# Performance work log

Measured on AMD Instinct MI355X. Metric: run time of the kernel, lower is better.

Reference implementation:

```python
import jax, jax.numpy as jnp
import numpy as np

H = 16   # n_heads == n_I
D = 64   # d_q = d_k = d_v = d_r
DX = H * D
B, S = 4, 2048

def setup_inputs() -> dict:
    key = jax.random.key(0)
    ks = jax.random.split(key, 9)
    sc = 0.02
    return {
        "value": jax.random.normal(ks[0], (B, S, DX), jnp.float32),
        "key":   jax.random.normal(ks[1], (B, S, DX), jnp.float32),
        "query": jax.random.normal(ks[2], (B, S, DX), jnp.float32),
        "Wq_w": jax.random.normal(ks[3], (DX, DX), jnp.float32) * sc,
        "Wq_b": jnp.zeros((DX,), jnp.float32),
        "Wk_w": jax.random.normal(ks[4], (DX, DX), jnp.float32) * sc,
        "Wk_b": jnp.zeros((DX,), jnp.float32),
        "Wv_w": jax.random.normal(ks[5], (DX, DX), jnp.float32) * sc,
        "Wv_b": jnp.zeros((DX,), jnp.float32),
        "Wr_w": jax.random.normal(ks[6], (DX, DX), jnp.float32) * sc,
        "Wr_b": jnp.zeros((DX,), jnp.float32),
        "Wout_w": jax.random.normal(ks[7], (DX, DX), jnp.float32) * sc,
        "Wout_b": jnp.zeros((DX,), jnp.float32),
    }

def _heads(x, b, s):
    # [b, s, H*D] -> [b, H, s, D]
    return x.reshape(b, s, H, D).transpose(0, 2, 1, 3)

def reference(value, key, query, Wq_w, Wq_b, Wk_w, Wk_b, Wv_w, Wv_b,
              Wr_w, Wr_b, Wout_w, Wout_b):
    b, s, _ = query.shape
    # torch nn.Linear: y = x @ W.T + b
    Q = _heads(query @ Wq_w.T + Wq_b, b, s)   # [b,H,s,D]
    K = _heads(key   @ Wk_w.T + Wk_b, b, s)
    V = _heads(value @ Wv_w.T + Wv_b, b, s)
    R = _heads(query @ Wr_w.T + Wr_b, b, s)
    dot_scale = jnp.sqrt(jnp.float32(D))
    scores = jnp.einsum("bhid,bhjd->bhij", Q, K) / dot_scale  # [b,H,s,s]
    attn = jax.nn.softmax(scores, axis=-1)                    # dropout p=0
    out = jnp.einsum("bhij,bhjd->bhid", attn, V)              # [b,H,s,D]
    out = out * R                                             # R-gating
    out = out.transpose(0, 2, 1, 3).reshape(b, s, H * D)
    return out @ Wout_w.T + Wout_b
```

## Files before the change

### kernel.cpp

```cpp
#include <hip/hip_runtime.h>
#include <hip/hip_bf16.h>

typedef __bf16 bf16;
typedef __bf16 bf16x4 __attribute__((ext_vector_type(4)));
typedef __bf16 bf16x8 __attribute__((ext_vector_type(8)));
typedef float  f32x4  __attribute__((ext_vector_type(4)));

#define MFMA_16x16x32(a, b, c) __builtin_amdgcn_mfma_f32_16x16x32_bf16((a), (b), (c), 0, 0, 0)

typedef const void __attribute__((address_space(1))) gvoid;
typedef void __attribute__((address_space(3))) svoid;

__device__ __forceinline__ void async_copy16(const void* gptr, void* ldsptr) {
    __builtin_amdgcn_global_load_lds((gvoid*)gptr, (svoid*)ldsptr, 16, 0, 0);
}

__device__ __forceinline__ int swz8(int row, int quad) {
    return (quad ^ ((row >> 1) & 3)) * 8;
}

__global__ void cvt3_acts(const float* __restrict__ s0, const float* __restrict__ s1,
                          const float* __restrict__ s2,
                          bf16* __restrict__ d0, bf16* __restrict__ d1, bf16* __restrict__ d2)
{
    constexpr int N4SEG = 8192 * 1024 / 4;
    int i = blockIdx.x * blockDim.x + threadIdx.x;
    const int stride = gridDim.x * blockDim.x;
    for (; i < 3 * N4SEG; i += stride) {
        const int seg = i / N4SEG;
        const int j = i - seg * N4SEG;
        const float* s = seg == 0 ? s0 : (seg == 1 ? s1 : s2);
        bf16* d = seg == 0 ? d0 : (seg == 1 ? d1 : d2);
        float4 v = ((const float4*)s)[j];
        bf16x4 o = { (bf16)v.x, (bf16)v.y, (bf16)v.z, (bf16)v.w };
        ((bf16x4*)d)[j] = o;
    }
}

__global__ void cvt5_wts(const float* __restrict__ s0, const float* __restrict__ s1,
                         const float* __restrict__ s2, const float* __restrict__ s3,
                         const float* __restrict__ s4,
                         bf16* __restrict__ d0, bf16* __restrict__ d1, bf16* __restrict__ d2,
                         bf16* __restrict__ d3, bf16* __restrict__ d4)
{
    constexpr int N4SEG = 1024 * 1024 / 4;
    int i = blockIdx.x * blockDim.x + threadIdx.x;
    const int stride = gridDim.x * blockDim.x;
    for (; i < 5 * N4SEG; i += stride) {
        const int seg = i / N4SEG;
        const int j = i - seg * N4SEG;
        const float* s = seg == 0 ? s0 : seg == 1 ? s1 : seg == 2 ? s2 : seg == 3 ? s3 : s4;
        bf16* d = seg == 0 ? d0 : seg == 1 ? d1 : seg == 2 ? d2 : seg == 3 ? d3 : d4;
        float4 v = ((const float4*)s)[j];
        bf16x4 o = { (bf16)v.x, (bf16)v.y, (bf16)v.z, (bf16)v.w };
        ((bf16x4*)d)[j] = o;
    }
}

__global__ void proj_fused(const bf16* __restrict__ xq, const bf16* __restrict__ xk,
                           const bf16* __restrict__ xv, const bf16* __restrict__ wall,
                           const float* __restrict__ ball,
                           bf16* __restrict__ qr, bf16* __restrict__ kws,
                           bf16* __restrict__ vtws)
{
    constexpr int K = 1024, SDIM = 2048;
    __shared__ alignas(16) bf16 As[128 * 32];
    __shared__ alignas(16) bf16 Bs[128 * 32];

    const int tid  = threadIdx.x;
    const int lane = tid & 63;
    const int wave = tid >> 6;
    const int wm   = wave >> 1;
    const int wn   = wave & 1;
    const int bm   = blockIdx.x * 128;
    const int by   = blockIdx.y;
    const int bn   = by * 128;
    const int l15  = lane & 15;
    const int quad = lane >> 4;

    const bf16* X = (by < 16) ? xq : (by < 24 ? xk : xv);

    const int srow = lane >> 2;
    const int scol = (lane & 3) * 8;

    const bf16* aseg0 = X + (size_t)(bm + wave * 32 + srow) * K + scol;
    const bf16* aseg1 = X + (size_t)(bm + wave * 32 + 16 + srow) * K + scol;
    const bf16* bseg0 = wall + (size_t)(bn + wave * 32 + srow) * K + scol;
    const bf16* bseg1 = wall + (size_t)(bn + wave * 32 + 16 + srow) * K + scol;
    bf16* as0 = As + (wave * 2 + 0) * 512;
    bf16* as1 = As + (wave * 2 + 1) * 512;
    bf16* bs0 = Bs + (wave * 2 + 0) * 512;
    bf16* bs1 = Bs + (wave * 2 + 1) * 512;

    f32x4 acc[4][4] = {};

    for (int k0 = 0; k0 < K; k0 += 32) {
        __syncthreads();
        async_copy16(aseg0 + k0, as0);
        async_copy16(aseg1 + k0, as1);
        async_copy16(bseg0 + k0, bs0);
        async_copy16(bseg1 + k0, bs1);
        __syncthreads();

        bf16x8 af[4], bfr[4];
        #pragma unroll
        for (int i = 0; i < 4; ++i)
            af[i] = *(const bf16x8*)(As + (wm * 64 + i * 16 + l15) * 32 + quad * 8);
        #pragma unroll
        for (int j = 0; j < 4; ++j)
            bfr[j] = *(const bf16x8*)(Bs + (wn * 64 + j * 16 + l15) * 32 + quad * 8);
        #pragma unroll
        for (int i = 0; i < 4; ++i)
            #pragma unroll
            for (int j = 0; j < 4; ++j)
                acc[i][j] = MFMA_16x16x32(af[i], bfr[j], acc[i][j]);
    }

    #pragma unroll
    for (int i = 0; i < 4; ++i) {
        const int rowg = bm + wm * 64 + i * 16 + quad * 4;
        #pragma unroll
        for (int j = 0; j < 4; ++j) {
            const int colg = bn + wn * 64 + j * 16 + l15;
            const float bv = ball[colg];
            if (by < 16) {
                #pragma unroll
                for (int r = 0; r < 4; ++r)
                    qr[(size_t)(rowg + r) * 2048 + colg] = (bf16)(acc[i][j][r] + bv);
            } else if (by < 24) {
                const int cl = colg - 2048;
                #pragma unroll
                for (int r = 0; r < 4; ++r)
                    kws[(size_t)(rowg + r) * 1024 + cl] = (bf16)(acc[i][j][r] + bv);
            } else {
                const int d = colg - 3072;
                bf16x4 o;
                #pragma unroll
                for (int r = 0; r < 4; ++r) o[r] = (bf16)(acc[i][j][r] + bv);
                *(bf16x4*)(vtws + (size_t)(rowg >> 11) * 1024 * SDIM
                                + (size_t)d * SDIM + (rowg & (SDIM - 1))) = o;
            }
        }
    }
}

__global__ void gemm_out(const bf16* __restrict__ X, const bf16* __restrict__ W,
                         const float* __restrict__ bias, float* __restrict__ Y)
{
    constexpr int K = 1024, N = 1024;
    __shared__ alignas(16) bf16 As[128 * 32];
    __shared__ alignas(16) bf16 Bs[128 * 32];

    const int tid  = threadIdx.x;
    const int lane = tid & 63;
    const int wave = tid >> 6;
    const int wm   = wave >> 1;
    const int wn   = wave & 1;
    const int bm   = blockIdx.x * 128;
    const int bn   = blockIdx.y * 128;
    const int l15  = lane & 15;
    const int quad = lane >> 4;

    const int srow = lane >> 2;
    const int scol = (lane & 3) * 8;

    const bf16* aseg0 = X + (size_t)(bm + wave * 32 + srow) * K + scol;
    const bf16* aseg1 = X + (size_t)(bm + wave * 32 + 16 + srow) * K + scol;
    const bf16* bseg0 = W + (size_t)(bn + wave * 32 + srow) * K + scol;
    const bf16* bseg1 = W + (size_t)(bn + wave * 32 + 16 + srow) * K + scol;
    bf16* as0 = As + (wave * 2 + 0) * 512;
    bf16* as1 = As + (wave * 2 + 1) * 512;
    bf16* bs0 = Bs + (wave * 2 + 0) * 512;
    bf16* bs1 = Bs + (wave * 2 + 1) * 512;

    f32x4 acc[4][4] = {};

    for (int k0 = 0; k0 < K; k0 += 32) {
        __syncthreads();
        async_copy16(aseg0 + k0, as0);
        async_copy16(aseg1 + k0, as1);
        async_copy16(bseg0 + k0, bs0);
        async_copy16(bseg1 + k0, bs1);
        __syncthreads();

        bf16x8 af[4], bfr[4];
        #pragma unroll
        for (int i = 0; i < 4; ++i)
            af[i] = *(const bf16x8*)(As + (wm * 64 + i * 16 + l15) * 32 + quad * 8);
        #pragma unroll
        for (int j = 0; j < 4; ++j)
            bfr[j] = *(const bf16x8*)(Bs + (wn * 64 + j * 16 + l15) * 32 + quad * 8);
        #pragma unroll
        for (int i = 0; i < 4; ++i)
            #pragma unroll
            for (int j = 0; j < 4; ++j)
                acc[i][j] = MFMA_16x16x32(af[i], bfr[j], acc[i][j]);
    }

    #pragma unroll
    for (int i = 0; i < 4; ++i) {
        const int rowg = bm + wm * 64 + i * 16 + quad * 4;
        #pragma unroll
        for (int j = 0; j < 4; ++j) {
            const int colg = bn + wn * 64 + j * 16 + l15;
            const float bv = bias[colg];
            #pragma unroll
            for (int r = 0; r < 4; ++r)
                Y[(size_t)(rowg + r) * N + colg] = acc[i][j][r] + bv;
        }
    }
}

__launch_bounds__(256, 4)
__global__ void attn_fused(const bf16* __restrict__ QRp, const bf16* __restrict__ Kp,
                           const bf16* __restrict__ Vtp, bf16* __restrict__ Op)
{
    constexpr int S = 2048, DXc = 1024, QRST = 2048, Dh = 64;
    constexpr int PST = 40;
    __shared__ alignas(16) bf16 KsLo[64 * 32], KsHi[64 * 32];
    __shared__ alignas(16) bf16 VtLo[64 * 32], VtHi[64 * 32];
    __shared__ alignas(16) bf16 Pt[4][2][2][16 * PST];

    const int tid  = threadIdx.x;
    const int lane = tid & 63;
    const int wave = tid >> 6;
    const int qt = blockIdx.x, h = blockIdx.y, b = blockIdx.z;
    const int l15  = lane & 15;
    const int quad = lane >> 4;

    const size_t qrbase = ((size_t)b * S) * QRST + h * Dh;
    const size_t kbase  = ((size_t)b * S) * DXc + h * Dh;
    const size_t vtbase = ((size_t)(b * 16 + h) * Dh) * S;
    const size_t obase  = ((size_t)b * S) * DXc + h * Dh;

    constexpr float QSCALE = 0.125f * 1.44269504088896340736f;
    bf16x8 qf[2][2];
    #pragma unroll
    for (int mi = 0; mi < 2; ++mi) {
        const int qrow = qt * 128 + wave * 32 + mi * 16 + l15;
        const bf16* qptr = QRp + qrbase + (size_t)qrow * QRST + quad * 8;
        qf[mi][0] = *(const bf16x8*)(qptr);
        qf[mi][1] = *(const bf16x8*)(qptr + 32);
        #pragma unroll
        for (int j = 0; j < 8; ++j) {
            qf[mi][0][j] = (bf16)((float)qf[mi][0][j] * QSCALE);
            qf[mi][1][j] = (bf16)((float)qf[mi][1][j] * QSCALE);
        }
    }

    bf16x8 onef;
    #pragma unroll
    for (int j = 0; j < 8; ++j) onef[j] = (bf16)1.0f;

    f32x4 oacc[2][4] = {};
    f32x4 lsacc[2] = {};

    const int srow = lane >> 2;
    const int scol = ((lane & 3) ^ ((srow >> 1) & 3)) * 8;
    const bf16* kseg = Kp  + kbase  + (size_t)(16 * wave + srow) * DXc + scol;
    const bf16* vseg = Vtp + vtbase + (size_t)(16 * wave + srow) * S   + scol;
    bf16* ksl = KsLo + wave * 512;
    bf16* ksh = KsHi + wave * 512;
    bf16* vtl = VtLo + wave * 512;
    bf16* vth = VtHi + wave * 512;

    for (int kv0 = 0; kv0 < S; kv0 += 64) {
        __syncthreads();
        async_copy16(kseg + (size_t)kv0 * DXc,      ksl);
        async_copy16(kseg + (size_t)kv0 * DXc + 32, ksh);
        async_copy16(vseg + kv0,                    vtl);
        async_copy16(vseg + kv0 + 32,               vth);
        __syncthreads();

        f32x4 st[2][4];
        #pragma unroll
        for (int nb = 0; nb < 4; ++nb) {
            bf16x8 kf0 = *(const bf16x8*)(KsLo + (nb * 16 + l15) * 32 + swz8(l15, quad));
            bf16x8 kf1 = *(const bf16x8*)(KsHi + (nb * 16 + l15) * 32 + swz8(l15, quad));
            #pragma unroll
            for (int mi = 0; mi < 2; ++mi) {
                f32x4 z = {0.f, 0.f, 0.f, 0.f};
                z = MFMA_16x16x32(kf1, qf[mi][1], z);
                st[mi][nb] = MFMA_16x16x32(kf0, qf[mi][0], z);
            }
        }
        #pragma unroll
        for (int mi = 0; mi < 2; ++mi) {
            #pragma unroll
            for (int nb = 0; nb < 4; ++nb) {
                bf16x4 pt;
                #pragma unroll
                for (int r = 0; r < 4; ++r) {
                    float p = __builtin_exp2f(st[mi][nb][r]);
                    pt[r] = (bf16)p;
                }
                *(bf16x4*)(&Pt[wave][mi][nb >> 1][0] + l15 * PST
                           + (nb & 1) * 16 + quad * 4) = pt;
            }
        }

        #pragma unroll
        for (int half = 0; half < 2; ++half) {
            const bf16* vb = half ? VtHi : VtLo;
            bf16x8 vtf[4];
            #pragma unroll
            for (int db = 0; db < 4; ++db)
                vtf[db] = *(const bf16x8*)(vb + (db * 16 + l15) * 32 + swz8(l15, quad));
            #pragma unroll
            for (int mi = 0; mi < 2; ++mi) {
                bf16x8 pf = *(const bf16x8*)(&Pt[wave][mi][half][0]
                                             + l15 * PST + quad * 8);
                #pragma unroll
                for (int db = 0; db < 4; ++db)
                    oacc[mi][db] = MFMA_16x16x32(vtf[db], pf, oacc[mi][db]);
                lsacc[mi] = MFMA_16x16x32(onef, pf, lsacc[mi]);
            }
        }
    }

    #pragma unroll
    for (int mi = 0; mi < 2; ++mi) {
        const float inv = 1.0f / lsacc[mi][0];
        const int qrow = qt * 128 + wave * 32 + mi * 16 + l15;
        const bf16* rrow = QRp + qrbase + (size_t)qrow * QRST + 1024;
        bf16* orow = Op + obase + (size_t)qrow * DXc;
        #pragma unroll
        for (int db = 0; db < 4; ++db) {
            bf16x4 rg = *(const bf16x4*)(rrow + db * 16 + quad * 4);
            bf16x4 o;
            #pragma unroll
            for (int r = 0; r < 4; ++r)
                o[r] = (bf16)(oacc[mi][db][r] * inv * (float)rg[r]);
            *(bf16x4*)(orow + db * 16 + quad * 4) = o;
        }
    }
}

extern "C" void kernel_launch(void* const* d_in, const int* in_sizes, int n_in,
                              void* d_out, int out_size, void* d_ws, size_t ws_size,
                              hipStream_t stream)
{
    (void)in_sizes; (void)n_in; (void)out_size; (void)ws_size;
    constexpr int B = 4, S = 2048, DX = 1024, M = B * S;
    constexpr size_t MD = (size_t)M * DX;
    constexpr size_t WD = (size_t)DX * DX;

    const float* value  = (const float*)d_in[0];
    const float* keyi   = (const float*)d_in[1];
    const float* query  = (const float*)d_in[2];
    const float* Wq_w   = (const float*)d_in[3];
    const float* Wq_b   = (const float*)d_in[4];
    const float* Wk_w   = (const float*)d_in[5];
    const float* Wk_b   = (const float*)d_in[6];
    const float* Wv_w   = (const float*)d_in[7];
    const float* Wv_b   = (const float*)d_in[8];
    const float* Wr_w   = (const float*)d_in[9];
    const float* Wr_b   = (const float*)d_in[10];
    const float* Wout_w = (const float*)d_in[11];
    const float* Wout_b = (const float*)d_in[12];

    bf16* p = (bf16*)d_ws;
    bf16* xv   = p;  p += MD;
    bf16* xk   = p;  p += MD;
    bf16* xq   = p;  p += MD;
    bf16* wall = p;  p += 4 * WD;
    bf16* wo   = p;  p += WD;
    bf16* qr   = p;  p += 2 * MD;
    bf16* kws  = p;  p += MD;
    bf16* vtws = p;  p += MD;
    float* ball = (float*)p;
    bf16* ows = xv;

    hipMemcpyAsync(ball,            Wq_b, DX * sizeof(float), hipMemcpyDeviceToDevice, stream);
    hipMemcpyAsync(ball + DX,       Wr_b, DX * sizeof(float), hipMemcpyDeviceToDevice, stream);
    hipMemcpyAsync(ball + 2 * DX,   Wk_b, DX * sizeof(float), hipMemcpyDeviceToDevice, stream);
    hipMemcpyAsync(ball + 3 * DX,   Wv_b, DX * sizeof(float), hipMemcpyDeviceToDevice, stream);

    cvt3_acts<<<dim3(2048), dim3(256), 0, stream>>>(value, keyi, query, xv, xk, xq);
    cvt5_wts <<<dim3(1024), dim3(256), 0, stream>>>(Wq_w, Wr_w, Wk_w, Wv_w, Wout_w,
                                                    wall, wall + WD, wall + 2 * WD,
                                                    wall + 3 * WD, wo);

    proj_fused<<<dim3(M / 128, 32), dim3(256), 0, stream>>>(
        xq, xk, xv, wall, ball, qr, kws, vtws);

    attn_fused<<<dim3(S / 128, 16, B), dim3(256), 0, stream>>>(qr, kws, vtws, ows);

    gemm_out<<<dim3(M / 128, DX / 128), dim3(256), 0, stream>>>(
        ows, wo, Wout_b, (float*)d_out);
}
```

Measured before the change: 398.7 us.

## Double-buffer LDS tiles in projection, output GEMM and attention loops

Converts the single-buffered LDS staging in proj_fused, gemm_out and attn_fused into ping-pong buffers. The next K/V or A/B tile is prefetched with async global-to-LDS copies before computing on the current one, and the loop now needs one barrier per iteration instead of two. The aim is to hide global load latency behind MFMA work and cut barrier stalls. In exchange, LDS use per block doubles for the staged tiles, which could limit occupancy.

```diff
diff --git a/kernel.cpp b/kernel.cpp
--- a/kernel.cpp
+++ b/kernel.cpp
@@ -64,8 +64,8 @@
                            bf16* __restrict__ vtws)
 {
     constexpr int K = 1024, SDIM = 2048;
-    __shared__ alignas(16) bf16 As[128 * 32];
-    __shared__ alignas(16) bf16 Bs[128 * 32];
+    __shared__ alignas(16) bf16 As[2][128 * 32];
+    __shared__ alignas(16) bf16 Bs[2][128 * 32];
 
     const int tid  = threadIdx.x;
     const int lane = tid & 63;
@@ -87,28 +87,38 @@
     const bf16* aseg1 = X + (size_t)(bm + wave * 32 + 16 + srow) * K + scol;
     const bf16* bseg0 = wall + (size_t)(bn + wave * 32 + srow) * K + scol;
     const bf16* bseg1 = wall + (size_t)(bn + wave * 32 + 16 + srow) * K + scol;
-    bf16* as0 = As + (wave * 2 + 0) * 512;
-    bf16* as1 = As + (wave * 2 + 1) * 512;
-    bf16* bs0 = Bs + (wave * 2 + 0) * 512;
-    bf16* bs1 = Bs + (wave * 2 + 1) * 512;
 
     f32x4 acc[4][4] = {};
 
+    {
+        bf16* as0 = As[0] + (wave * 2 + 0) * 512;
+        bf16* as1 = As[0] + (wave * 2 + 1) * 512;
+        bf16* bs0 = Bs[0] + (wave * 2 + 0) * 512;
+        bf16* bs1 = Bs[0] + (wave * 2 + 1) * 512;
+        async_copy16(aseg0, as0);
+        async_copy16(aseg1, as1);
+        async_copy16(bseg0, bs0);
+        async_copy16(bseg1, bs1);
+    }
+
     for (int k0 = 0; k0 < K; k0 += 32) {
+        const int cur = (k0 >> 5) & 1;
         __syncthreads();
-        async_copy16(aseg0 + k0, as0);
-        async_copy16(aseg1 + k0, as1);
-        async_copy16(bseg0 + k0, bs0);
-        async_copy16(bseg1 + k0, bs1);
-        __syncthreads();
+        if (k0 + 32 < K) {
+            const int nxt = cur ^ 1;
+            async_copy16(aseg0 + k0 + 32, As[nxt] + (wave * 2 + 0) * 512);
+            async_copy16(aseg1 + k0 + 32, As[nxt] + (wave * 2 + 1) * 512);
+            async_copy16(bseg0 + k0 + 32, Bs[nxt] + (wave * 2 + 0) * 512);
+            async_copy16(bseg1 + k0 + 32, Bs[nxt] + (wave * 2 + 1) * 512);
+        }
 
         bf16x8 af[4], bfr[4];
         #pragma unroll
         for (int i = 0; i < 4; ++i)
-            af[i] = *(const bf16x8*)(As + (wm * 64 + i * 16 + l15) * 32 + quad * 8);
+            af[i] = *(const bf16x8*)(As[cur] + (wm * 64 + i * 16 + l15) * 32 + quad * 8);
         #pragma unroll
         for (int j = 0; j < 4; ++j)
-            bfr[j] = *(const bf16x8*)(Bs + (wn * 64 + j * 16 + l15) * 32 + quad * 8);
+            bfr[j] = *(const bf16x8*)(Bs[cur] + (wn * 64 + j * 16 + l15) * 32 + quad * 8);
         #pragma unroll
         for (int i = 0; i < 4; ++i)
             #pragma unroll
@@ -148,8 +158,8 @@
                          const float* __restrict__ bias, float* __restrict__ Y)
 {
     constexpr int K = 1024, N = 1024;
-    __shared__ alignas(16) bf16 As[128 * 32];
-    __shared__ alignas(16) bf16 Bs[128 * 32];
+    __shared__ alignas(16) bf16 As[2][128 * 32];
+    __shared__ alignas(16) bf16 Bs[2][128 * 32];
 
     const int tid  = threadIdx.x;
     const int lane = tid & 63;
@@ -168,28 +178,34 @@
     const bf16* aseg1 = X + (size_t)(bm + wave * 32 + 16 + srow) * K + scol;
     const bf16* bseg0 = W + (size_t)(bn + wave * 32 + srow) * K + scol;
     const bf16* bseg1 = W + (size_t)(bn + wave * 32 + 16 + srow) * K + scol;
-    bf16* as0 = As + (wave * 2 + 0) * 512;
-    bf16* as1 = As + (wave * 2 + 1) * 512;
-    bf16* bs0 = Bs + (wave * 2 + 0) * 512;
-    bf16* bs1 = Bs + (wave * 2 + 1) * 512;
 
     f32x4 acc[4][4] = {};
 
+    {
+        async_copy16(aseg0, As[0] + (wave * 2 + 0) * 512);
+        async_copy16(aseg1, As[0] + (wave * 2 + 1) * 512);
+        async_copy16(bseg0, Bs[0] + (wave * 2 + 0) * 512);
+        async_copy16(bseg1, Bs[0] + (wave * 2 + 1) * 512);
+    }
+
     for (int k0 = 0; k0 < K; k0 += 32) {
+        const int cur = (k0 >> 5) & 1;
         __syncthreads();
-        async_copy16(aseg0 + k0, as0);
-        async_copy16(aseg1 + k0, as1);
-        async_copy16(bseg0 + k0, bs0);
-        async_copy16(bseg1 + k0, bs1);
-        __syncthreads();
+        if (k0 + 32 < K) {
+            const int nxt = cur ^ 1;
+            async_copy16(aseg0 + k0 + 32, As[nxt] + (wave * 2 + 0) * 512);
+            async_copy16(aseg1 + k0 + 32, As[nxt] + (wave * 2 + 1) * 512);
+            async_copy16(bseg0 + k0 + 32, Bs[nxt] + (wave * 2 + 0) * 512);
+            async_copy16(bseg1 + k0 + 32, Bs[nxt] + (wave * 2 + 1) * 512);
+        }
 
         bf16x8 af[4], bfr[4];
         #pragma unroll
         for (int i = 0; i < 4; ++i)
-            af[i] = *(const bf16x8*)(As + (wm * 64 + i * 16 + l15) * 32 + quad * 8);
+            af[i] = *(const bf16x8*)(As[cur] + (wm * 64 + i * 16 + l15) * 32 + quad * 8);
         #pragma unroll
         for (int j = 0; j < 4; ++j)
-            bfr[j] = *(const bf16x8*)(Bs + (wn * 64 + j * 16 + l15) * 32 + quad * 8);
+            bfr[j] = *(const bf16x8*)(Bs[cur] + (wn * 64 + j * 16 + l15) * 32 + quad * 8);
         #pragma unroll
         for (int i = 0; i < 4; ++i)
             #pragma unroll
@@ -217,8 +233,8 @@
 {
     constexpr int S = 2048, DXc = 1024, QRST = 2048, Dh = 64;
     constexpr int PST = 40;
-    __shared__ alignas(16) bf16 KsLo[64 * 32], KsHi[64 * 32];
-    __shared__ alignas(16) bf16 VtLo[64 * 32], VtHi[64 * 32];
+    __shared__ alignas(16) bf16 Ks[2][2][64 * 32];
+    __shared__ alignas(16) bf16 Vt[2][2][64 * 32];
     __shared__ alignas(16) bf16 Pt[4][2][2][16 * PST];
 
     const int tid  = threadIdx.x;
@@ -232,6 +248,17 @@
     const size_t kbase  = ((size_t)b * S) * DXc + h * Dh;
     const size_t vtbase = ((size_t)(b * 16 + h) * Dh) * S;
     const size_t obase  = ((size_t)b * S) * DXc + h * Dh;
+
+    const int srow = lane >> 2;
+    const int scol = ((lane & 3) ^ ((srow >> 1) & 3)) * 8;
+    const bf16* kseg = Kp  + kbase  + (size_t)(16 * wave + srow) * DXc + scol;
+    const bf16* vseg = Vtp + vtbase + (size_t)(16 * wave + srow) * S   + scol;
+    const int soff = wave * 512;
+
+    async_copy16(kseg,      &Ks[0][0][soff]);
+    async_copy16(kseg + 32, &Ks[0][1][soff]);
+    async_copy16(vseg,      &Vt[0][0][soff]);
+    async_copy16(vseg + 32, &Vt[0][1][soff]);
 
     constexpr float QSCALE = 0.125f * 1.44269504088896340736f;
     bf16x8 qf[2][2];
@@ -255,28 +282,24 @@
     f32x4 oacc[2][4] = {};
     f32x4 lsacc[2] = {};
 
-    const int srow = lane >> 2;
-    const int scol = ((lane & 3) ^ ((srow >> 1) & 3)) * 8;
-    const bf16* kseg = Kp  + kbase  + (size_t)(16 * wave + srow) * DXc + scol;
-    const bf16* vseg = Vtp + vtbase + (size_t)(16 * wave + srow) * S   + scol;
-    bf16* ksl = KsLo + wave * 512;
-    bf16* ksh = KsHi + wave * 512;
-    bf16* vtl = VtLo + wave * 512;
-    bf16* vth = VtHi + wave * 512;
-
-    for (int kv0 = 0; kv0 < S; kv0 += 64) {
+    for (int t = 0; t < S / 64; ++t) {
+        const int cur = t & 1;
         __syncthreads();
-        async_copy16(kseg + (size_t)kv0 * DXc,      ksl);
-        async_copy16(kseg + (size_t)kv0 * DXc + 32, ksh);
-        async_copy16(vseg + kv0,                    vtl);
-        async_copy16(vseg + kv0 + 32,               vth);
-        __syncthreads();
+        if (t + 1 < S / 64) {
+            const int nxt = cur ^ 1;
+            const size_t ko = (size_t)(t + 1) * 64 * DXc;
+            const int    vo = (t + 1) * 64;
+            async_copy16(kseg + ko,      &Ks[nxt][0][soff]);
+            async_copy16(kseg + ko + 32, &Ks[nxt][1][soff]);
+            async_copy16(vseg + vo,      &Vt[nxt][0][soff]);
+            async_copy16(vseg + vo + 32, &Vt[nxt][1][soff]);
+        }
 
         f32x4 st[2][4];
         #pragma unroll
         for (int nb = 0; nb < 4; ++nb) {
-            bf16x8 kf0 = *(const bf16x8*)(KsLo + (nb * 16 + l15) * 32 + swz8(l15, quad));
-            bf16x8 kf1 = *(const bf16x8*)(KsHi + (nb * 16 + l15) * 32 + swz8(l15, quad));
+            bf16x8 kf0 = *(const bf16x8*)(&Ks[cur][0][0] + (nb * 16 + l15) * 32 + swz8(l15, quad));
+            bf16x8 kf1 = *(const bf16x8*)(&Ks[cur][1][0] + (nb * 16 + l15) * 32 + swz8(l15, quad));
             #pragma unroll
             for (int mi = 0; mi < 2; ++mi) {
                 f32x4 z = {0.f, 0.f, 0.f, 0.f};
@@ -301,7 +324,7 @@
 
         #pragma unroll
         for (int half = 0; half < 2; ++half) {
-            const bf16* vb = half ? VtHi : VtLo;
+            const bf16* vb = &Vt[cur][half][0];
             bf16x8 vtf[4];
             #pragma unroll
             for (int db = 0; db < 4; ++db)
```

Result: slower. 410.4 us (+3.0%).
